# Kernel optimization log

Hardware: AMD Instinct MI355X
Metric: run time of the kernel (lower is better)

Reference implementation:

```python
import jax, jax.numpy as jnp
import numpy as np

VIOL_TOL = 12.0
CLASH_TOL = 1.5
C_N_LEN = (1.329, 1.341)        # (non-proline, proline)
C_N_STD = (0.014, 0.016)
CA_C_N = (-0.5203, 0.0353)      # (gt cos, stddev)
C_N_CA = (-0.4473, 0.0311)
EPS = 1e-6


def setup_inputs() -> dict:
    key = jax.random.key(0)
    k = jax.random.split(key, 6)
    B, N = 1, 512
    pos = jax.random.normal(k[0], (B, N, 14, 3), jnp.float32) * 5.0
    atom_mask = jnp.ones((B, N, 14), jnp.float32)
    residue_types = jax.random.randint(k[1], (B, N), 0, 21, dtype=jnp.int32)
    residue_index = jnp.broadcast_to(jnp.arange(N, dtype=jnp.int32)[None], (B, N))
    vdw_table = jax.random.uniform(k[2], (21, 14), jnp.float32, 1.0, 2.0)
    lower_bound_table = jax.random.uniform(k[3], (21, 14, 14), jnp.float32, 1.0, 2.0)
    upper_bound_table = lower_bound_table + jax.random.uniform(k[4], (21, 14, 14), jnp.float32, 0.5, 1.5)
    return {
        'predicted_positions': pos,
        'atom_mask': atom_mask,
        'residue_types': residue_types,
        'residue_index': residue_index,
        'vdw_table': vdw_table,
        'lower_bound_table': lower_bound_table,
        'upper_bound_table': upper_bound_table,
    }


def _bond_angle_losses(pos, atom_mask, residue_types, residue_index):
    f32 = pos.dtype
    this_ca, this_ca_m = pos[:, :-1, 1, :], atom_mask[:, :-1, 1]
    this_c, this_c_m = pos[:, :-1, 2, :], atom_mask[:, :-1, 2]
    next_n, next_n_m = pos[:, 1:, 0, :], atom_mask[:, 1:, 0]
    next_ca, next_ca_m = pos[:, 1:, 1, :], atom_mask[:, 1:, 1]
    no_gap = (residue_index[:, 1:] - residue_index[:, :-1] == 1).astype(f32)

    c_n_len = jnp.sqrt(jnp.sum((this_c - next_n) ** 2, -1) + EPS)
    pro = (residue_types[:, 1:] == 14).astype(f32)
    gt_len = (1.0 - pro) * C_N_LEN[0] + pro * C_N_LEN[1]
    gt_std = (1.0 - pro) * C_N_STD[0] + pro * C_N_STD[1]
    c_n_mask = this_c_m * next_n_m * no_gap
    c_n_err = jnp.sqrt((c_n_len - gt_len) ** 2 + EPS)
    c_n_loss = jnp.sum(c_n_mask * jax.nn.relu(c_n_err - VIOL_TOL * gt_std), -1) / (jnp.sum(c_n_mask, -1) + EPS)

    ca_c_len = jnp.sqrt(jnp.sum((this_ca - this_c) ** 2, -1) + EPS)
    n_ca_len = jnp.sqrt(jnp.sum((next_n - next_ca) ** 2, -1) + EPS)
    c_ca_u = (this_ca - this_c) / ca_c_len[..., None]
    c_n_u = (next_n - this_c) / c_n_len[..., None]
    n_ca_u = (next_ca - next_n) / n_ca_len[..., None]

    ca_c_n = jnp.sum(c_ca_u * c_n_u, -1)
    ca_c_n_mask = this_ca_m * this_c_m * next_n_m * no_gap
    ca_c_n_err = jnp.sqrt((ca_c_n - CA_C_N[0]) ** 2 + EPS)
    ca_c_n_loss = jnp.sum(ca_c_n_mask * jax.nn.relu(ca_c_n_err - VIOL_TOL * CA_C_N[1]), -1) / (jnp.sum(ca_c_n_mask, -1) + EPS)

    c_n_ca = jnp.sum(-c_n_u * n_ca_u, -1)
    c_n_ca_mask = this_c_m * next_n_m * next_ca_m * no_gap
    c_n_ca_err = jnp.sqrt((c_n_ca - C_N_CA[0]) ** 2 + EPS)
    c_n_ca_loss = jnp.sum(c_n_ca_mask * jax.nn.relu(c_n_ca_err - VIOL_TOL * C_N_CA[1]), -1) / (jnp.sum(c_n_ca_mask, -1) + EPS)

    return c_n_loss, ca_c_n_loss, c_n_ca_loss


def _clash_per_atom(pos, atom_mask, residue_types, residue_index, vdw_table):
    f32 = pos.dtype
    B, N = pos.shape[:2]
    A = N * 14
    pos_f = pos.reshape(B, A, 3)
    m_f = atom_mask.reshape(B, A)
    rt = jnp.minimum(residue_types, 20)
    vdw_f = vdw_table[rt].reshape(B, A)  # gather [B,N,14] -> flat

    diff = pos_f[:, :, None, :] - pos_f[:, None, :, :]
    dist = jnp.sqrt(jnp.sum(diff ** 2, -1) + 1e-8)  # [B,A,A]

    pair = m_f[:, :, None] * m_f[:, None, :]
    ari = jnp.repeat(residue_index, 14, axis=1)  # atom residue index [B,A]
    pair = pair * (ari[:, :, None] < ari[:, None, :]).astype(f32)

    slot = jnp.tile(jnp.arange(14), N)[None]  # [1,A]
    rtf = jnp.repeat(residue_types, 14, axis=1)
    c_n_bond = ((slot[:, :, None] == 2) & (slot[:, None, :] == 0) & (ari[:, None, :] - ari[:, :, None] == 1)) | \
               ((slot[:, :, None] == 0) & (slot[:, None, :] == 2) & (ari[:, :, None] - ari[:, None, :] == 1))
    disulfide = (rtf[:, :, None] == 4) & (rtf[:, None, :] == 4) & (slot[:, :, None] == 5) & (slot[:, None, :] == 5)
    pair = pair * (~c_n_bond).astype(f32) * (~disulfide).astype(f32)

    vdw_sum = vdw_f[:, :, None] + vdw_f[:, None, :]
    clash = jax.nn.relu(vdw_sum - CLASH_TOL - dist) * pair
    per_atom = (jnp.sum(clash, axis=1) + jnp.sum(clash, axis=2)).reshape(B, N, 14)
    return per_atom


def _within_per_atom(pos, atom_mask, residue_types, lower_bound_table, upper_bound_table):
    f32 = pos.dtype
    rt = jnp.minimum(residue_types, 20)
    lb = lower_bound_table[rt]  # [B,N,14,14]
    ub = upper_bound_table[rt]
    d = jnp.sqrt(jnp.sum((pos[:, :, :, None, :] - pos[:, :, None, :, :]) ** 2, -1) + 1e-8)
    pair = atom_mask[:, :, :, None] * atom_mask[:, :, None, :]
    pair = pair * (1.0 - jnp.eye(14, dtype=f32)[None, None])
    pair = pair * ((lb > 0.0) | (ub > 0.0)).astype(f32)
    loss = (jax.nn.relu(lb - d) + jax.nn.relu(d - ub)) * pair
    return jnp.sum(loss, axis=-2) + jnp.sum(loss, axis=-1)  # [B,N,14]


def reference(predicted_positions, atom_mask, residue_types, residue_index,
              vdw_table, lower_bound_table, upper_bound_table):
    c_n, ca_c_n, c_n_ca = _bond_angle_losses(predicted_positions, atom_mask, residue_types, residue_index)
    clash_pa = _clash_per_atom(predicted_positions, atom_mask, residue_types, residue_index, vdw_table)
    within_pa = _within_per_atom(predicted_positions, atom_mask, residue_types, lower_bound_table, upper_bound_table)
    num_atoms = jnp.clip(jnp.sum(atom_mask, axis=(1, 2)), 1e-6, None)
    clash_loss = jnp.sum(clash_pa + within_pa, axis=(1, 2)) / num_atoms
    return c_n + ca_c_n + c_n_ca + clash_loss
```

## Files before the change

### kernel.cpp

```cpp
#include <hip/hip_runtime.h>

#define EPS 1e-6f
#define JT 256
#define WB 56

static __device__ __forceinline__ float wave_reduce_add(float v) {
#pragma unroll
    for (int o = 32; o > 0; o >>= 1) v += __shfl_down(v, o, 64);
    return v;
}


__device__ void do_bonds(const float* __restrict__ P, const float* __restrict__ M,
                         const int* __restrict__ RT, const int* __restrict__ RI,
                         float* __restrict__ Wtail, int N) {
    float n0 = 0.f, de0 = 0.f, n1 = 0.f, de1 = 0.f, n2 = 0.f, de2 = 0.f;
    for (int i = threadIdx.x; i < N - 1; i += blockDim.x) {
        float no_gap = (RI[i + 1] - RI[i] == 1) ? 1.f : 0.f;
        const float* ca0 = P + i * 42 + 3;
        const float* c0  = P + i * 42 + 6;
        const float* nn  = P + (i + 1) * 42 + 0;
        const float* ca1 = P + (i + 1) * 42 + 3;
        float m_ca0 = M[i * 14 + 1], m_c0 = M[i * 14 + 2];
        float m_nn = M[(i + 1) * 14 + 0], m_ca1 = M[(i + 1) * 14 + 1];

        float bx = nn[0] - c0[0], by = nn[1] - c0[1], bz = nn[2] - c0[2];
        float c_n_len = sqrtf(bx * bx + by * by + bz * bz + EPS);
        float pro = (RT[i + 1] == 14) ? 1.f : 0.f;
        float gt_len = (1.f - pro) * 1.329f + pro * 1.341f;
        float gt_std = (1.f - pro) * 0.014f + pro * 0.016f;
        float cnm = m_c0 * m_nn * no_gap;
        float dl = c_n_len - gt_len;
        float cne = sqrtf(dl * dl + EPS);
        n0 += cnm * fmaxf(cne - 12.f * gt_std, 0.f);
        de0 += cnm;

        float ax = ca0[0] - c0[0], ay = ca0[1] - c0[1], az = ca0[2] - c0[2];
        float ca_c_len = sqrtf(ax * ax + ay * ay + az * az + EPS);
        float ex = ca1[0] - nn[0], ey = ca1[1] - nn[1], ez = ca1[2] - nn[2];
        float n_ca_len = sqrtf(ex * ex + ey * ey + ez * ez + EPS);
        float inv_cn = 1.f / c_n_len, inv_ac = 1.f / ca_c_len, inv_nc = 1.f / n_ca_len;
        float ux = bx * inv_cn, uy = by * inv_cn, uz = bz * inv_cn;
        float cx = ax * inv_ac, cy = ay * inv_ac, cz = az * inv_ac;
        float wx = ex * inv_nc, wy = ey * inv_nc, wz = ez * inv_nc;

        float cacn = cx * ux + cy * uy + cz * uz;
        float m1 = m_ca0 * m_c0 * m_nn * no_gap;
        float t1 = cacn + 0.5203f;
        float e1 = sqrtf(t1 * t1 + EPS);
        n1 += m1 * fmaxf(e1 - 12.f * 0.0353f, 0.f);
        de1 += m1;

        float cnca = -(ux * wx + uy * wy + uz * wz);
        float m2 = m_c0 * m_nn * m_ca1 * no_gap;
        float t2 = cnca + 0.4473f;
        float e2 = sqrtf(t2 * t2 + EPS);
        n2 += m2 * fmaxf(e2 - 12.f * 0.0311f, 0.f);
        de2 += m2;
    }
    n0 = wave_reduce_add(n0); de0 = wave_reduce_add(de0);
    n1 = wave_reduce_add(n1); de1 = wave_reduce_add(de1);
    n2 = wave_reduce_add(n2); de2 = wave_reduce_add(de2);
    __shared__ float red[24];
    int lane = threadIdx.x & 63, wid = threadIdx.x >> 6;
    if (lane == 0) {
        red[wid * 6 + 0] = n0; red[wid * 6 + 1] = de0; red[wid * 6 + 2] = n1;
        red[wid * 6 + 3] = de1; red[wid * 6 + 4] = n2; red[wid * 6 + 5] = de2;
    }
    __syncthreads();
    if (threadIdx.x < 6) {
        Wtail[threadIdx.x] = red[threadIdx.x] + red[6 + threadIdx.x]
                           + red[12 + threadIdx.x] + red[18 + threadIdx.x];
    }
}

__device__ void do_within(const float* __restrict__ pos, const float* __restrict__ am,
                          const int* __restrict__ rtypes,
                          const float* __restrict__ lbt, const float* __restrict__ ubt,
                          float* __restrict__ slot, int N, int b, int wblk) {
    int total = N * 196;
    float sum = 0.f;
    for (int idx = wblk * blockDim.x + threadIdx.x; idx < total; idx += WB * blockDim.x) {
        int n = idx / 196;
        int p = idx - n * 196;
        int i = p / 14;
        int j = p - i * 14;
        if (i == j) continue;
        size_t bn = (size_t)b * N + n;
        int rt = rtypes[bn]; rt = rt < 20 ? rt : 20;
        const float* pi = pos + bn * 42 + i * 3;
        const float* pj = pos + bn * 42 + j * 3;
        float dx = pi[0] - pj[0], dy = pi[1] - pj[1], dz = pi[2] - pj[2];
        float d = sqrtf(dx * dx + dy * dy + dz * dz + 1e-8f);
        float lb = lbt[rt * 196 + p], ub = ubt[rt * 196 + p];
        float gate = (lb > 0.f || ub > 0.f) ? 1.f : 0.f;
        float m = am[bn * 14 + i] * am[bn * 14 + j] * gate;
        sum += (fmaxf(lb - d, 0.f) + fmaxf(d - ub, 0.f)) * m;
    }
    sum = wave_reduce_add(sum);
    __shared__ float red2[4];
    int lane = threadIdx.x & 63, wid = threadIdx.x >> 6;
    if (lane == 0) red2[wid] = sum;
    __syncthreads();
    if (threadIdx.x == 0) *slot = red2[0] + red2[1] + red2[2] + red2[3];
}

__device__ void do_clash(const float* __restrict__ P, const float* __restrict__ M,
                         const int* __restrict__ RT, const int* __restrict__ RI,
                         const float* __restrict__ vdw, float* __restrict__ slot,
                         int N, int A, int T, int p) {
    int bi = (int)floorf(((float)(2 * T + 1)
                - sqrtf((float)((2 * T + 1) * (2 * T + 1) - 8 * p))) * 0.5f);
    bi = bi < 0 ? 0 : (bi >= T ? T - 1 : bi);
    while (bi + 1 <= T - 1 && ((bi + 1) * T - (bi + 1) * bi / 2) <= p) ++bi;
    while ((bi * T - bi * (bi - 1) / 2) > p) --bi;
    int bj = bi + (p - (bi * T - bi * (bi - 1) / 2));

    __shared__ float4 sPos[JT];
    __shared__ float sMask[JT];
    __shared__ int sRI[JT];
    __shared__ int sMeta[JT];

    int t = threadIdx.x;
    int j = bj * JT + t;
    if (j < A) {
        int res = j / 14;
        int sl = j - res * 14;
        int rt = RT[res];
        int rtc = rt < 20 ? rt : 20;
        sPos[t] = make_float4(P[j * 3], P[j * 3 + 1], P[j * 3 + 2], vdw[rtc * 14 + sl]);
        sMask[t] = M[j];
        sRI[t] = RI[res];
        sMeta[t] = sl | (((rt == 4) && (sl == 5)) ? 16 : 0);
    } else {
        sPos[t] = make_float4(1e30f, 1e30f, 1e30f, -1e30f);
        sMask[t] = 0.f; sRI[t] = 0x7fffffff; sMeta[t] = 0;
    }
    __syncthreads();

    int i = bi * JT + t;
    float sum = 0.f;
    if (i < A) {
        int res = i / 14;
        int isl = i - res * 14;
        int irt = RT[res];
        int rtc = irt < 20 ? irt : 20;
        float vis = vdw[rtc * 14 + isl] - 1.5f;
        float xi = P[i * 3], yi = P[i * 3 + 1], zi = P[i * 3 + 2];
        float mi = M[i];
        int iri = RI[res];
        bool icys = (irt == 4) && (isl == 5);
        if (mi != 0.f) {
            for (int base = 0; base < JT; base += 8) {
                float4 r[8];
#pragma unroll
                for (int k = 0; k < 8; ++k) r[k] = sPos[base + k];
#pragma unroll
                for (int k = 0; k < 8; ++k) {
                    float dx = xi - r[k].x, dy = yi - r[k].y, dz = zi - r[k].z;
                    float d2 = dx * dx + dy * dy + dz * dz + 1e-8f;
                    float s = vis + r[k].w;
                    if (d2 < s * s && s > 0.f) {
                        int jj = base + k;
                        int jg = bj * JT + jj;
                        if (i < jg) {
                            int jri = sRI[jj];
                            if (iri != jri) {
                                int dj = jri - iri;
                                int jmeta = sMeta[jj];
                                int jsl = jmeta & 15;
                                bool cn = (isl == 2 && jsl == 0 && dj == 1) ||
                                          (isl == 0 && jsl == 2 && dj == -1);
                                bool ssb = icys && (jmeta & 16);
                                if (!cn && !ssb) {
                                    sum += (s - sqrtf(d2)) * mi * sMask[jj];
                                }
                            }
                        }
                    }
                }
            }
        }
    }
    sum = wave_reduce_add(sum);
    __shared__ float red3[4];
    int lane = t & 63, wid = t >> 6;
    if (lane == 0) red3[wid] = sum;
    __syncthreads();
    if (t == 0) *slot = red3[0] + red3[1] + red3[2] + red3[3];
}

__global__ __launch_bounds__(JT) void main_kernel(
        const float* __restrict__ pos, const float* __restrict__ am,
        const int* __restrict__ rtypes, const int* __restrict__ rindex,
        const float* __restrict__ vdw, const float* __restrict__ lbt,
        const float* __restrict__ ubt, float* __restrict__ ws,
        int N, int A, int T, int CB, int NBP, int stride) {
    int b = blockIdx.y;
    const float* P = pos + (size_t)b * A * 3;
    const float* M = am + (size_t)b * A;
    const int* RT = rtypes + (size_t)b * N;
    const int* RI = rindex + (size_t)b * N;
    float* W = ws + (size_t)b * stride;
    int bid = blockIdx.x;
    if (bid < CB) {
        do_clash(P, M, RT, RI, vdw, &W[bid], N, A, T, bid);
    } else if (bid < NBP) {
        do_within(pos, am, rtypes, lbt, ubt, &W[bid], N, b, bid - CB);
    } else {
        do_bonds(P, M, RT, RI, &W[NBP], N);
    }
}

__global__ __launch_bounds__(256) void final_kernel(
        const float* __restrict__ am, const float* __restrict__ ws,
        float* __restrict__ out, int N, int NBP, int stride) {
    int b = blockIdx.x;
    const float* M = am + (size_t)b * N * 14;
    const float* W = ws + (size_t)b * stride;
    float s = 0.f, pairs = 0.f;
    for (int i = threadIdx.x; i < N * 14; i += blockDim.x) s += M[i];
    for (int i = threadIdx.x; i < NBP; i += blockDim.x) pairs += W[i];
    s = wave_reduce_add(s);
    pairs = wave_reduce_add(pairs);
    __shared__ float red[8];
    int lane = threadIdx.x & 63, wid = threadIdx.x >> 6;
    if (lane == 0) { red[wid] = s; red[4 + wid] = pairs; }
    __syncthreads();
    if (threadIdx.x == 0) {
        float na = fmaxf(red[0] + red[1] + red[2] + red[3], 1e-6f);
        float P2 = red[4] + red[5] + red[6] + red[7];
        const float* T6 = W + NBP;
        float loss = T6[0] / (T6[1] + EPS) + T6[2] / (T6[3] + EPS)
                   + T6[4] / (T6[5] + EPS) + 2.f * P2 / na;
        out[b] = loss;
    }
}

extern "C" void kernel_launch(void* const* d_in, const int* in_sizes, int n_in,
                              void* d_out, int out_size, void* d_ws, size_t ws_size,
                              hipStream_t stream) {
    const float* pos = (const float*)d_in[0];
    const float* am = (const float*)d_in[1];
    const int* rtypes = (const int*)d_in[2];
    const int* rindex = (const int*)d_in[3];
    const float* vdw = (const float*)d_in[4];
    const float* lbt = (const float*)d_in[5];
    const float* ubt = (const float*)d_in[6];
    float* out = (float*)d_out;
    float* ws = (float*)d_ws;

    int B = out_size;
    int N = in_sizes[2] / B;
    int A = N * 14;
    int T = (A + JT - 1) / JT;
    int CB = T * (T + 1) / 2;
    int NBP = CB + WB;
    int stride = NBP + 6;

    dim3 grid(NBP + 1, B);
    main_kernel<<<grid, JT, 0, stream>>>(pos, am, rtypes, rindex, vdw, lbt, ubt,
                                         ws, N, A, T, CB, NBP, stride);
    final_kernel<<<B, 256, 0, stream>>>(am, ws, out, N, NBP, stride);
}
```

Measured before the change: 101.9 us.

## Retile clash pairs into 512x64 rectangular tiles with two i-atoms per thread

The triangular 256x256 clash tiling becomes rectangular tiles of 512 i-atoms by 64 j-atoms, and each thread now handles two i-atoms against each shared j entry. This gives more, smaller blocks for better load balance across CUs, reuses each shared-memory load for two pairs, and drops the sqrt-based tile index decode. The 1.5 offset is folded into the j-side vdw, masked i-atoms are disabled through their radius, launch bounds request 4 blocks per CU, and the final mask sum uses float4 loads. In exchange, diagonal tiles do more wasted pair tests, and each block's preload and reduction are spread over less work.

New measurement: 89.59 us. 1.14x faster.

```diff
diff --git a/kernel.cpp b/kernel.cpp
--- a/kernel.cpp
+++ b/kernel.cpp
@@ -1,8 +1,10 @@
 #include <hip/hip_runtime.h>
 
 #define EPS 1e-6f
-#define JT 256
-#define WB 56
+#define IT 512
+#define JTL 64
+#define RATIO 8
+#define WB 64
 
 static __device__ __forceinline__ float wave_reduce_add(float v) {
 #pragma unroll
@@ -108,74 +110,110 @@
 __device__ void do_clash(const float* __restrict__ P, const float* __restrict__ M,
                          const int* __restrict__ RT, const int* __restrict__ RI,
                          const float* __restrict__ vdw, float* __restrict__ slot,
-                         int N, int A, int T, int p) {
-    int bi = (int)floorf(((float)(2 * T + 1)
-                - sqrtf((float)((2 * T + 1) * (2 * T + 1) - 8 * p))) * 0.5f);
-    bi = bi < 0 ? 0 : (bi >= T ? T - 1 : bi);
-    while (bi + 1 <= T - 1 && ((bi + 1) * T - (bi + 1) * bi / 2) <= p) ++bi;
-    while ((bi * T - bi * (bi - 1) / 2) > p) --bi;
-    int bj = bi + (p - (bi * T - bi * (bi - 1) / 2));
-
-    __shared__ float4 sPos[JT];
-    __shared__ float sMask[JT];
-    __shared__ int sRI[JT];
-    __shared__ int sMeta[JT];
+                         int N, int A, int TJ, int p) {
+    int bi = 0, rem = p;
+    while (true) {
+        int cnt = TJ - RATIO * bi;
+        cnt = cnt > 0 ? cnt : 0;
+        if (rem < cnt) break;
+        rem -= cnt; ++bi;
+    }
+    int bj = RATIO * bi + rem;
+
+    __shared__ float4 sPos[JTL];
+    __shared__ float sMask[JTL];
+    __shared__ int sRI[JTL];
+    __shared__ int sMeta[JTL];
 
     int t = threadIdx.x;
-    int j = bj * JT + t;
-    if (j < A) {
-        int res = j / 14;
-        int sl = j - res * 14;
-        int rt = RT[res];
-        int rtc = rt < 20 ? rt : 20;
-        sPos[t] = make_float4(P[j * 3], P[j * 3 + 1], P[j * 3 + 2], vdw[rtc * 14 + sl]);
-        sMask[t] = M[j];
-        sRI[t] = RI[res];
-        sMeta[t] = sl | (((rt == 4) && (sl == 5)) ? 16 : 0);
-    } else {
-        sPos[t] = make_float4(1e30f, 1e30f, 1e30f, -1e30f);
-        sMask[t] = 0.f; sRI[t] = 0x7fffffff; sMeta[t] = 0;
-    }
-    __syncthreads();
-
-    int i = bi * JT + t;
+    if (t < JTL) {
+        int j = bj * JTL + t;
+        if (j < A) {
+            int res = j / 14;
+            int sl = j - res * 14;
+            int rt = RT[res];
+            int rtc = rt < 20 ? rt : 20;
+            sPos[t] = make_float4(P[j * 3], P[j * 3 + 1], P[j * 3 + 2],
+                                  vdw[rtc * 14 + sl] - 1.5f);
+            sMask[t] = M[j];
+            sRI[t] = RI[res];
+            sMeta[t] = sl | (((rt == 4) && (sl == 5)) ? 16 : 0);
+        } else {
+            sPos[t] = make_float4(1e30f, 1e30f, 1e30f, -1e30f);
+            sMask[t] = 0.f; sRI[t] = 0x7fffffff; sMeta[t] = 0;
+        }
+    }
+    __syncthreads();
+
+    int i0 = bi * IT + t;
+    int i1 = i0 + 256;
+    float xi0 = 0.f, yi0 = 0.f, zi0 = 0.f, vi0 = -1e30f, mi0 = 0.f;
+    float xi1 = 0.f, yi1 = 0.f, zi1 = 0.f, vi1 = -1e30f, mi1 = 0.f;
+    int iri0 = 0, iri1 = 0;
+    bool icys0 = false, icys1 = false;
+    int isl0 = -1, isl1 = -1;
+    if (i0 < A) {
+        int res = i0 / 14; isl0 = i0 - res * 14;
+        int rt = RT[res]; int rtc = rt < 20 ? rt : 20;
+        vi0 = vdw[rtc * 14 + isl0];
+        xi0 = P[i0 * 3]; yi0 = P[i0 * 3 + 1]; zi0 = P[i0 * 3 + 2];
+        mi0 = M[i0]; iri0 = RI[res]; icys0 = (rt == 4) && (isl0 == 5);
+        if (mi0 == 0.f) vi0 = -1e30f;
+    }
+    if (i1 < A) {
+        int res = i1 / 14; isl1 = i1 - res * 14;
+        int rt = RT[res]; int rtc = rt < 20 ? rt : 20;
+        vi1 = vdw[rtc * 14 + isl1];
+        xi1 = P[i1 * 3]; yi1 = P[i1 * 3 + 1]; zi1 = P[i1 * 3 + 2];
+        mi1 = M[i1]; iri1 = RI[res]; icys1 = (rt == 4) && (isl1 == 5);
+        if (mi1 == 0.f) vi1 = -1e30f;
+    }
+
     float sum = 0.f;
-    if (i < A) {
-        int res = i / 14;
-        int isl = i - res * 14;
-        int irt = RT[res];
-        int rtc = irt < 20 ? irt : 20;
-        float vis = vdw[rtc * 14 + isl] - 1.5f;
-        float xi = P[i * 3], yi = P[i * 3 + 1], zi = P[i * 3 + 2];
-        float mi = M[i];
-        int iri = RI[res];
-        bool icys = (irt == 4) && (isl == 5);
-        if (mi != 0.f) {
-            for (int base = 0; base < JT; base += 8) {
-                float4 r[8];
+    int jbase_g = bj * JTL;
+    for (int base = 0; base < JTL; base += 8) {
+        float4 r[8];
 #pragma unroll
-                for (int k = 0; k < 8; ++k) r[k] = sPos[base + k];
+        for (int k = 0; k < 8; ++k) r[k] = sPos[base + k];
 #pragma unroll
-                for (int k = 0; k < 8; ++k) {
-                    float dx = xi - r[k].x, dy = yi - r[k].y, dz = zi - r[k].z;
-                    float d2 = dx * dx + dy * dy + dz * dz + 1e-8f;
-                    float s = vis + r[k].w;
-                    if (d2 < s * s && s > 0.f) {
-                        int jj = base + k;
-                        int jg = bj * JT + jj;
-                        if (i < jg) {
-                            int jri = sRI[jj];
-                            if (iri != jri) {
-                                int dj = jri - iri;
-                                int jmeta = sMeta[jj];
-                                int jsl = jmeta & 15;
-                                bool cn = (isl == 2 && jsl == 0 && dj == 1) ||
-                                          (isl == 0 && jsl == 2 && dj == -1);
-                                bool ssb = icys && (jmeta & 16);
-                                if (!cn && !ssb) {
-                                    sum += (s - sqrtf(d2)) * mi * sMask[jj];
-                                }
-                            }
+        for (int k = 0; k < 8; ++k) {
+            float w = r[k].w;
+            {
+                float dx = xi0 - r[k].x, dy = yi0 - r[k].y, dz = zi0 - r[k].z;
+                float d2 = dx * dx + dy * dy + dz * dz;
+                float s = vi0 + w;
+                if (s > 0.f && d2 < s * s) {
+                    int jj = base + k, jg = jbase_g + jj;
+                    if (i0 < jg) {
+                        int jri = sRI[jj];
+                        if (iri0 != jri) {
+                            int dj = jri - iri0;
+                            int jm = sMeta[jj], jsl = jm & 15;
+                            bool cn = (isl0 == 2 && jsl == 0 && dj == 1) ||
+                                      (isl0 == 0 && jsl == 2 && dj == -1);
+                            bool ssb = icys0 && (jm & 16);
+                            if (!cn && !ssb)
+                                sum += (s - sqrtf(d2 + 1e-8f)) * mi0 * sMask[jj];
+                        }
+                    }
+                }
+            }
+            {
+                float dx = xi1 - r[k].x, dy = yi1 - r[k].y, dz = zi1 - r[k].z;
+                float d2 = dx * dx + dy * dy + dz * dz;
+                float s = vi1 + w;
+                if (s > 0.f && d2 < s * s) {
+                    int jj = base + k, jg = jbase_g + jj;
+                    if (i1 < jg) {
+                        int jri = sRI[jj];
+                        if (iri1 != jri) {
+                            int dj = jri - iri1;
+                            int jm = sMeta[jj], jsl = jm & 15;
+                            bool cn = (isl1 == 2 && jsl == 0 && dj == 1) ||
+                                      (isl1 == 0 && jsl == 2 && dj == -1);
+                            bool ssb = icys1 && (jm & 16);
+                            if (!cn && !ssb)
+                                sum += (s - sqrtf(d2 + 1e-8f)) * mi1 * sMask[jj];
                         }
                     }
                 }
@@ -190,12 +228,12 @@
     if (t == 0) *slot = red3[0] + red3[1] + red3[2] + red3[3];
 }
 
-__global__ __launch_bounds__(JT) void main_kernel(
+__global__ __launch_bounds__(256, 4) void main_kernel(
         const float* __restrict__ pos, const float* __restrict__ am,
         const int* __restrict__ rtypes, const int* __restrict__ rindex,
         const float* __restrict__ vdw, const float* __restrict__ lbt,
         const float* __restrict__ ubt, float* __restrict__ ws,
-        int N, int A, int T, int CB, int NBP, int stride) {
+        int N, int A, int TJ, int CB, int NBP, int stride) {
     int b = blockIdx.y;
     const float* P = pos + (size_t)b * A * 3;
     const float* M = am + (size_t)b * A;
@@ -204,7 +242,7 @@
     float* W = ws + (size_t)b * stride;
     int bid = blockIdx.x;
     if (bid < CB) {
-        do_clash(P, M, RT, RI, vdw, &W[bid], N, A, T, bid);
+        do_clash(P, M, RT, RI, vdw, &W[bid], N, A, TJ, bid);
     } else if (bid < NBP) {
         do_within(pos, am, rtypes, lbt, ubt, &W[bid], N, b, bid - CB);
     } else {
@@ -219,7 +257,14 @@
     const float* M = am + (size_t)b * N * 14;
     const float* W = ws + (size_t)b * stride;
     float s = 0.f, pairs = 0.f;
-    for (int i = threadIdx.x; i < N * 14; i += blockDim.x) s += M[i];
+    int A = N * 14;
+    int A4 = A >> 2;
+    const float4* M4 = (const float4*)M;
+    for (int i = threadIdx.x; i < A4; i += blockDim.x) {
+        float4 v = M4[i];
+        s += v.x + v.y + v.z + v.w;
+    }
+    for (int i = A4 << 2; i < A; ++i) if (threadIdx.x == 0) s += M[i];
     for (int i = threadIdx.x; i < NBP; i += blockDim.x) pairs += W[i];
     s = wave_reduce_add(s);
     pairs = wave_reduce_add(pairs);
@@ -253,13 +298,18 @@
     int B = out_size;
     int N = in_sizes[2] / B;
     int A = N * 14;
-    int T = (A + JT - 1) / JT;
-    int CB = T * (T + 1) / 2;
+    int TI = (A + IT - 1) / IT;
+    int TJ = (A + JTL - 1) / JTL;
+    int CB = 0;
+    for (int bi = 0; bi < TI; ++bi) {
+        int c = TJ - RATIO * bi;
+        if (c > 0) CB += c;
+    }
     int NBP = CB + WB;
     int stride = NBP + 6;
 
     dim3 grid(NBP + 1, B);
-    main_kernel<<<grid, JT, 0, stream>>>(pos, am, rtypes, rindex, vdw, lbt, ubt,
-                                         ws, N, A, T, CB, NBP, stride);
+    main_kernel<<<grid, 256, 0, stream>>>(pos, am, rtypes, rindex, vdw, lbt, ubt,
+                                          ws, N, A, TJ, CB, NBP, stride);
     final_kernel<<<B, 256, 0, stream>>>(am, ws, out, N, NBP, stride);
 }
```
